# Optimization experiments

Measured on AMD Instinct MI355X. Metric: run time of the kernel, lower is better.

The kernel has to match this reference:

```python
import jax, jax.numpy as jnp
import numpy as np

N, LATENT, K, C = 50000, 16, 16, 64
BATCH = 4
MU = 2.0
HOT_TEMP = 0.01  # sigmoid temperature in hotness()


def _linear_init(key, out_dim, in_dim):
    s = 1.0 / np.sqrt(in_dim)
    kw, kb = jax.random.split(key)
    w = jax.random.uniform(kw, (out_dim, in_dim), jnp.float32, -s, s)
    b = jax.random.uniform(kb, (out_dim,), jnp.float32, -s, s)
    return w, b


def setup_inputs() -> dict:
    key = jax.random.key(0)
    ks = jax.random.split(key, 10)
    x = jax.random.normal(ks[0], (BATCH, N), jnp.float32)
    neighbour_id = jax.random.randint(ks[1], (N, K), 0, N)
    neighbour_distance = jax.random.uniform(ks[2], (N, K), jnp.float32)
    # self-neighbor at distance 0 (as in a real kNN table); keeps window sums > 0
    neighbour_distance = neighbour_distance.at[:, 0].set(0.0)
    clustering_labels = jax.random.randint(ks[3], (N,), 0, C)
    enc1_w, enc1_b = _linear_init(ks[4], 200, N)
    enc2_w, enc2_b = _linear_init(ks[5], LATENT, 200)
    dec_w, dec_b = _linear_init(ks[6], N, LATENT)
    h0_w, h0_b = _linear_init(ks[7], 200, LATENT)
    h1_w, h1_b = _linear_init(ks[8], 200, 200)
    h2_w, h2_b = _linear_init(ks[9], C, 200)
    B = jnp.array([1.0], jnp.float32)  # learnable bandwidth scale, B0=1.0
    return dict(x=x, neighbour_id=neighbour_id, neighbour_distance=neighbour_distance,
                clustering_labels=clustering_labels, enc1_w=enc1_w, enc1_b=enc1_b,
                enc2_w=enc2_w, enc2_b=enc2_b, dec_w=dec_w, dec_b=dec_b,
                h0_w=h0_w, h0_b=h0_b, h1_w=h1_w, h1_b=h1_b, h2_w=h2_w, h2_b=h2_b, B=B)


def reference(x, neighbour_id, neighbour_distance, clustering_labels,
              enc1_w, enc1_b, enc2_w, enc2_b, dec_w, dec_b,
              h0_w, h0_b, h1_w, h1_b, h2_w, h2_b, B):
    # ---- encode: Linear(N,200) -> sigmoid -> Linear(200,n)
    h = jax.nn.sigmoid(x @ enc1_w.T + enc1_b)
    encoded = h @ enc2_w.T + enc2_b                      # [b, n]

    # ---- hotness MLP (SiLU hidden layers, soft sigmoid output), batched over b
    z = encoded @ h0_w.T + h0_b
    z = z * jax.nn.sigmoid(z)
    z = z @ h1_w.T + h1_b
    z = z * jax.nn.sigmoid(z)
    z = z @ h2_w.T + h2_b                                # [b, C]
    H_cluster = jax.nn.sigmoid(HOT_TEMP * z)             # 1/(1+exp(-0.01 z))
    H = H_cluster[:, clustering_labels]                  # [b, N]

    # ---- per-mode bandwidths: (1 - H/2)^i * B,  i = 0..n-1
    powers = jnp.arange(LATENT, dtype=jnp.float32)[:, None]   # [n, 1]
    w = (1.0 - H[:, None, :] / 2.0) ** powers * B[0]          # [b, n, N]

    # ---- bubble window over K neighbours, normalized over K
    d2 = neighbour_distance ** 2                              # [N, K]
    denom = (w * MU) ** 2                                     # [b, n, N]
    win = jax.nn.relu(1.0 - d2[None, None] / denom[..., None])  # [b, n, N, K]
    win = win / jnp.sum(win, axis=-1, keepdims=True)

    # ---- convolve decoder basis (decoder.weight.T is [n, N]) with window
    basis_nbrs = dec_w.T[:, neighbour_id]                     # [n, N, K] gather
    convolved = jnp.einsum('bnik,nik->bni', win, basis_nbrs)  # [b, n, N]

    # ---- decode: bmm(encoded[b,1,n], convolved[b,n,N]) + bias
    out = jnp.einsum('bn,bni->bi', encoded, convolved) + dec_b  # [b, N]
    return out
```

## Files before the change

kernel.cpp:

```cpp
#include <hip/hip_runtime.h>
#include <math.h>

#define NPTS 50000
#define KNBR 16
#define LAT  16
#define NCLS 64
#define NB   4

#define ENC1_CHUNKS 5
#define ENC1_BLOCKS (200 * ENC1_CHUNKS)
#define NLANES (NPTS * 4)
#define CONV_BLOCKS ((NLANES + 255) / 256)

__device__ __forceinline__ float sigmoidf_(float v) { return 1.0f / (1.0f + expf(-v)); }

__global__ __launch_bounds__(256) void k_enc1(const float* __restrict__ x,
                                              const float* __restrict__ w,
                                              float* __restrict__ part) {
  const int NV4 = NPTS / 4;
  const int CV  = NV4 / ENC1_CHUNKS;
  int bid = blockIdx.x;
  int j = bid / ENC1_CHUNKS;
  int chunk = bid - j * ENC1_CHUNKS;
  int t = threadIdx.x;
  const float4* wv = (const float4*)(w + (size_t)j * NPTS);
  const float4* xv = (const float4*)x;
  float a0 = 0.f, a1 = 0.f, a2 = 0.f, a3 = 0.f;
  int vend = (chunk + 1) * CV;
#pragma unroll 2
  for (int v = chunk * CV + t; v < vend; v += 256) {
    float4 wf = wv[v];
    float4 x0 = xv[v];
    float4 x1 = xv[NV4 + v];
    float4 x2 = xv[2 * NV4 + v];
    float4 x3 = xv[3 * NV4 + v];
    a0 += wf.x * x0.x + wf.y * x0.y + wf.z * x0.z + wf.w * x0.w;
    a1 += wf.x * x1.x + wf.y * x1.y + wf.z * x1.z + wf.w * x1.w;
    a2 += wf.x * x2.x + wf.y * x2.y + wf.z * x2.z + wf.w * x2.w;
    a3 += wf.x * x3.x + wf.y * x3.y + wf.z * x3.z + wf.w * x3.w;
  }
#pragma unroll
  for (int off = 32; off > 0; off >>= 1) {
    a0 += __shfl_down(a0, off);
    a1 += __shfl_down(a1, off);
    a2 += __shfl_down(a2, off);
    a3 += __shfl_down(a3, off);
  }
  __shared__ float red[4][4];
  int wid = t >> 6;
  if ((t & 63) == 0) {
    red[wid][0] = a0; red[wid][1] = a1; red[wid][2] = a2; red[wid][3] = a3;
  }
  __syncthreads();
  if (t < 4) {
    float s = red[0][t] + red[1][t] + red[2][t] + red[3][t];
    part[j * 20 + chunk * 4 + t] = s;
  }
}

__global__ __launch_bounds__(1024) void k_mlpABC(const float* __restrict__ part,
                                                 const float* __restrict__ enc1_b,
                                                 const float* __restrict__ enc2_w,
                                                 const float* __restrict__ enc2_b,
                                                 const float* __restrict__ h0_w,
                                                 const float* __restrict__ h0_b,
                                                 float* __restrict__ w_enc,
                                                 float* __restrict__ z0g) {
  __shared__ float s_h[NB][200];
  __shared__ float s_enc[NB][LAT];
  int t = threadIdx.x;

  if (t < 800) {
    int j = t >> 2, b = t & 3;
    float v = part[j * 20 + 0 + b] + part[j * 20 + 4 + b] + part[j * 20 + 8 + b] +
              part[j * 20 + 12 + b] + part[j * 20 + 16 + b] + enc1_b[j];
    s_h[b][j] = sigmoidf_(v);
  }
  __syncthreads();

  {
    int g = t >> 4, p = t & 15;
    int b = g >> 4, i = g & 15;
    const float4* w4 = (const float4*)(enc2_w + i * 200);
    float s = 0.f;
    for (int f = p; f < 50; f += 16) {
      float4 w = w4[f];
      int j = f * 4;
      s += w.x * s_h[b][j] + w.y * s_h[b][j + 1] + w.z * s_h[b][j + 2] + w.w * s_h[b][j + 3];
    }
    s += __shfl_xor(s, 1, 16);
    s += __shfl_xor(s, 2, 16);
    s += __shfl_xor(s, 4, 16);
    s += __shfl_xor(s, 8, 16);
    if (p == 0) {
      s += enc2_b[i];
      s_enc[b][i] = s;
      w_enc[b * LAT + i] = s;
    }
  }
  __syncthreads();

  if (t < 800) {
    int jo = t >> 2, b = t & 3;
    const float4* hw = (const float4*)(h0_w + jo * LAT);
    float4 w0 = hw[0], w1 = hw[1], w2 = hw[2], w3 = hw[3];
    float s = h0_b[jo];
    s += w0.x * s_enc[b][0] + w0.y * s_enc[b][1] + w0.z * s_enc[b][2] + w0.w * s_enc[b][3];
    s += w1.x * s_enc[b][4] + w1.y * s_enc[b][5] + w1.z * s_enc[b][6] + w1.w * s_enc[b][7];
    s += w2.x * s_enc[b][8] + w2.y * s_enc[b][9] + w2.z * s_enc[b][10] + w2.w * s_enc[b][11];
    s += w3.x * s_enc[b][12] + w3.y * s_enc[b][13] + w3.z * s_enc[b][14] + w3.w * s_enc[b][15];
    z0g[jo * 4 + b] = s * sigmoidf_(s);
  }
}

__global__ __launch_bounds__(256) void k_mlpD(const float* __restrict__ z0g,
                                              const float* __restrict__ h1_w,
                                              const float* __restrict__ h1_b,
                                              float* __restrict__ z1g) {
  __shared__ __align__(16) float4 s_z0[200];
  int t = threadIdx.x;
  for (int o = t; o < 200; o += 256) s_z0[o] = ((const float4*)z0g)[o];
  __syncthreads();

  int row = blockIdx.x * 4 + (t >> 6);
  int l = t & 63;
  float d0 = 0.f, d1 = 0.f, d2 = 0.f, d3 = 0.f;
  if (l < 50) {
    float4 w = ((const float4*)(h1_w + row * 200))[l];
    float4 z0 = s_z0[4 * l + 0], z1 = s_z0[4 * l + 1];
    float4 z2 = s_z0[4 * l + 2], z3 = s_z0[4 * l + 3];
    d0 = w.x * z0.x + w.y * z1.x + w.z * z2.x + w.w * z3.x;
    d1 = w.x * z0.y + w.y * z1.y + w.z * z2.y + w.w * z3.y;
    d2 = w.x * z0.z + w.y * z1.z + w.z * z2.z + w.w * z3.z;
    d3 = w.x * z0.w + w.y * z1.w + w.z * z2.w + w.w * z3.w;
  }
#pragma unroll
  for (int m = 32; m > 0; m >>= 1) {
    d0 += __shfl_xor(d0, m, 64);
    d1 += __shfl_xor(d1, m, 64);
    d2 += __shfl_xor(d2, m, 64);
    d3 += __shfl_xor(d3, m, 64);
  }
  if (l == 0) {
    float bb = h1_b[row];
    float s;
    s = d0 + bb; z1g[row * 4 + 0] = s * sigmoidf_(s);
    s = d1 + bb; z1g[row * 4 + 1] = s * sigmoidf_(s);
    s = d2 + bb; z1g[row * 4 + 2] = s * sigmoidf_(s);
    s = d3 + bb; z1g[row * 4 + 3] = s * sigmoidf_(s);
  }
}

__global__ __launch_bounds__(256) void k_mlpE(const float* __restrict__ z1g,
                                              const float* __restrict__ h2_w,
                                              const float* __restrict__ h2_b,
                                              float* __restrict__ w_hcl) {
  __shared__ __align__(16) float4 s_z1[200];
  int t = threadIdx.x;
  for (int o = t; o < 200; o += 256) s_z1[o] = ((const float4*)z1g)[o];
  __syncthreads();

  int c = blockIdx.x * 4 + (t >> 6);
  int l = t & 63;
  float e0 = 0.f, e1 = 0.f, e2 = 0.f, e3 = 0.f;
  if (l < 50) {
    float4 w = ((const float4*)(h2_w + c * 200))[l];
    float4 za = s_z1[4 * l + 0], zb = s_z1[4 * l + 1];
    float4 zc = s_z1[4 * l + 2], zd = s_z1[4 * l + 3];
    e0 = w.x * za.x + w.y * zb.x + w.z * zc.x + w.w * zd.x;
    e1 = w.x * za.y + w.y * zb.y + w.z * zc.y + w.w * zd.y;
    e2 = w.x * za.z + w.y * zb.z + w.z * zc.z + w.w * zd.z;
    e3 = w.x * za.w + w.y * zb.w + w.z * zc.w + w.w * zd.w;
  }
#pragma unroll
  for (int m = 32; m > 0; m >>= 1) {
    e0 += __shfl_xor(e0, m, 64);
    e1 += __shfl_xor(e1, m, 64);
    e2 += __shfl_xor(e2, m, 64);
    e3 += __shfl_xor(e3, m, 64);
  }
  if (l == 0) {
    float sb = h2_b[c];
    w_hcl[0 * NCLS + c] = sigmoidf_(0.01f * (e0 + sb));
    w_hcl[1 * NCLS + c] = sigmoidf_(0.01f * (e1 + sb));
    w_hcl[2 * NCLS + c] = sigmoidf_(0.01f * (e2 + sb));
    w_hcl[3 * NCLS + c] = sigmoidf_(0.01f * (e3 + sb));
  }
}

__global__ __launch_bounds__(256) void k_conv(const int* __restrict__ nid,
                                              const float* __restrict__ nd,
                                              const int* __restrict__ labels,
                                              const float* __restrict__ dec_w,
                                              const float* __restrict__ dec_b,
                                              const float* __restrict__ Bp,
                                              const float* __restrict__ w_enc,
                                              const float* __restrict__ w_hcl,
                                              float* __restrict__ out) {
  __shared__ float s_enc[NB * LAT];
  __shared__ float s_hcl[NB * NCLS];
  int t = threadIdx.x;
  if (t < NB * LAT) s_enc[t] = w_enc[t];
  s_hcl[t] = w_hcl[t];
  __syncthreads();

  int gidx = blockIdx.x * 256 + t;
  int n = gidx >> 2;
  int q = t & 3;
  if (n >= NPTS) return;

  const float4* nd4 = (const float4*)nd + (size_t)n * 4;
  const int4*   ni4 = (const int4*)nid + (size_t)n * 4;
  float dA[16];
  int nA[16];
#pragma unroll
  for (int a = 0; a < 4; ++a) {
    float4 v = nd4[a];
    int4  iv = ni4[a];
    dA[a * 4 + 0] = v.x * v.x; dA[a * 4 + 1] = v.y * v.y;
    dA[a * 4 + 2] = v.z * v.z; dA[a * 4 + 3] = v.w * v.w;
    nA[a * 4 + 0] = iv.x; nA[a * 4 + 1] = iv.y;
    nA[a * 4 + 2] = iv.z; nA[a * 4 + 3] = iv.w;
  }

  int lab = labels[n];
  float decb = dec_b[n];
  float Bv = Bp[0];

  const float4* dw4 = (const float4*)dec_w;
  float4 dwp[8];
#pragma unroll
  for (int k = 0; k < 8; ++k)
    dwp[k] = dw4[(size_t)nA[k] * 4 + q];

  float inv0 = 1.0f / (4.0f * Bv * Bv);

  float ivd[4][4];
#pragma unroll
  for (int b = 0; b < 4; ++b) {
    float H = s_hcl[b * NCLS + lab];
    float base = 1.0f - 0.5f * H;
    float rb = __builtin_amdgcn_rcpf(base * base);
    float rb2 = rb * rb;
    float rb4 = rb2 * rb2;
    float rb8 = rb4 * rb4;
    float start = inv0;
    if (q & 1) start *= rb4;
    if (q & 2) start *= rb8;
    ivd[b][0] = start;
    ivd[b][1] = ivd[b][0] * rb;
    ivd[b][2] = ivd[b][1] * rb;
    ivd[b][3] = ivd[b][2] * rb;
  }

  float sden[4][4], num[4][4];
#pragma unroll
  for (int b = 0; b < 4; ++b)
#pragma unroll
    for (int j = 0; j < 4; ++j) { sden[b][j] = 0.f; num[b][j] = 0.f; }

#pragma unroll
  for (int k = 0; k < KNBR; ++k) {
    float4 dw = (k < 8) ? dwp[k] : dw4[(size_t)nA[k] * 4 + q];
    float d2k = dA[k];
#pragma unroll
    for (int b = 0; b < 4; ++b) {
      float w0 = fmaxf(fmaf(-d2k, ivd[b][0], 1.0f), 0.0f);
      float w1 = fmaxf(fmaf(-d2k, ivd[b][1], 1.0f), 0.0f);
      float w2 = fmaxf(fmaf(-d2k, ivd[b][2], 1.0f), 0.0f);
      float w3 = fmaxf(fmaf(-d2k, ivd[b][3], 1.0f), 0.0f);
      sden[b][0] += w0; num[b][0] = fmaf(w0, dw.x, num[b][0]);
      sden[b][1] += w1; num[b][1] = fmaf(w1, dw.y, num[b][1]);
      sden[b][2] += w2; num[b][2] = fmaf(w2, dw.z, num[b][2]);
      sden[b][3] += w3; num[b][3] = fmaf(w3, dw.w, num[b][3]);
    }
  }

  float acc[4];
#pragma unroll
  for (int b = 0; b < 4; ++b) {
    float a = 0.f;
#pragma unroll
    for (int j = 0; j < 4; ++j) {
      a = fmaf(s_enc[b * LAT + q * 4 + j] * __builtin_amdgcn_rcpf(sden[b][j]),
               num[b][j], a);
    }
    acc[b] = a;
  }

  float tA = (q & 1) ? acc[0] : acc[2];
  float tB = (q & 1) ? acc[1] : acc[3];
  float rA = __shfl_xor(tA, 1, 4);
  float rB = __shfl_xor(tB, 1, 4);
  float u = (q & 1) ? (acc[2] + rA) : (acc[0] + rA);
  float v = (q & 1) ? (acc[3] + rB) : (acc[1] + rB);
  float tC = (q & 2) ? u : v;
  float rC = __shfl_xor(tC, 2, 4);
  float f = (q & 2) ? (v + rC) : (u + rC);
  int bmap = ((q & 1) << 1) | ((q & 2) >> 1);
  out[(size_t)bmap * NPTS + n] = f + decb;
}

extern "C" void kernel_launch(void* const* d_in, const int* in_sizes, int n_in,
                              void* d_out, int out_size, void* d_ws, size_t ws_size,
                              hipStream_t stream) {
  const float* x      = (const float*)d_in[0];
  const int*   nid    = (const int*)d_in[1];
  const float* nd     = (const float*)d_in[2];
  const int*   labels = (const int*)d_in[3];
  const float* enc1_w = (const float*)d_in[4];
  const float* enc1_b = (const float*)d_in[5];
  const float* enc2_w = (const float*)d_in[6];
  const float* enc2_b = (const float*)d_in[7];
  const float* dec_w  = (const float*)d_in[8];
  const float* dec_b  = (const float*)d_in[9];
  const float* h0_w   = (const float*)d_in[10];
  const float* h0_b   = (const float*)d_in[11];
  const float* h1_w   = (const float*)d_in[12];
  const float* h1_b   = (const float*)d_in[13];
  const float* h2_w   = (const float*)d_in[14];
  const float* h2_b   = (const float*)d_in[15];
  const float* Bp     = (const float*)d_in[16];
  float* out = (float*)d_out;
  float* ws  = (float*)d_ws;
  float* part  = ws;
  float* w_enc = ws + 4000;
  float* w_hcl = ws + 4064;
  float* z0g   = ws + 4320;
  float* z1g   = ws + 5120;

  k_enc1<<<ENC1_BLOCKS, 256, 0, stream>>>(x, enc1_w, part);
  k_mlpABC<<<1, 1024, 0, stream>>>(part, enc1_b, enc2_w, enc2_b, h0_w, h0_b,
                                   w_enc, z0g);
  k_mlpD<<<50, 256, 0, stream>>>(z0g, h1_w, h1_b, z1g);
  k_mlpE<<<16, 256, 0, stream>>>(z1g, h2_w, h2_b, w_hcl);
  k_conv<<<CONV_BLOCKS, 256, 0, stream>>>(nid, nd, labels, dec_w, dec_b,
                                          Bp, w_enc, w_hcl, out);
}
```

Measured before the change: 37.76 us.

## Fuse small MLP kernels by recomputing early layers per block and final layer in conv

Merges the three small MLP launches (enc2+h0, h1, h2) into fewer kernels. Each of the 50 h1 blocks recomputes enc2 and h0 redundantly, and every conv block recomputes the h2 layer plus the hotness sigmoid from z1 before its main work. This removes two kernel launches and their serial dependency gaps. The cost is redundant arithmetic and extra h2_w reads in each of roughly 800 conv blocks.

```diff
diff --git a/kernel.cpp b/kernel.cpp
--- a/kernel.cpp
+++ b/kernel.cpp
@@ -58,20 +58,23 @@
   }
 }
 
-__global__ __launch_bounds__(1024) void k_mlpABC(const float* __restrict__ part,
-                                                 const float* __restrict__ enc1_b,
-                                                 const float* __restrict__ enc2_w,
-                                                 const float* __restrict__ enc2_b,
-                                                 const float* __restrict__ h0_w,
-                                                 const float* __restrict__ h0_b,
-                                                 float* __restrict__ w_enc,
-                                                 float* __restrict__ z0g) {
+__global__ __launch_bounds__(256) void k_mlpX(const float* __restrict__ part,
+                                              const float* __restrict__ enc1_b,
+                                              const float* __restrict__ enc2_w,
+                                              const float* __restrict__ enc2_b,
+                                              const float* __restrict__ h0_w,
+                                              const float* __restrict__ h0_b,
+                                              const float* __restrict__ h1_w,
+                                              const float* __restrict__ h1_b,
+                                              float* __restrict__ w_enc,
+                                              float* __restrict__ z1g) {
   __shared__ float s_h[NB][200];
   __shared__ float s_enc[NB][LAT];
+  __shared__ __align__(16) float s_z0t[200][NB];
   int t = threadIdx.x;
 
-  if (t < 800) {
-    int j = t >> 2, b = t & 3;
+  for (int o = t; o < 800; o += 256) {
+    int j = o >> 2, b = o & 3;
     float v = part[j * 20 + 0 + b] + part[j * 20 + 4 + b] + part[j * 20 + 8 + b] +
               part[j * 20 + 12 + b] + part[j * 20 + 16 + b] + enc1_b[j];
     s_h[b][j] = sigmoidf_(v);
@@ -79,29 +82,27 @@
   __syncthreads();
 
   {
-    int g = t >> 4, p = t & 15;
+    int g = t >> 2, p = t & 3;
     int b = g >> 4, i = g & 15;
     const float4* w4 = (const float4*)(enc2_w + i * 200);
     float s = 0.f;
-    for (int f = p; f < 50; f += 16) {
+    for (int f = p; f < 50; f += 4) {
       float4 w = w4[f];
       int j = f * 4;
       s += w.x * s_h[b][j] + w.y * s_h[b][j + 1] + w.z * s_h[b][j + 2] + w.w * s_h[b][j + 3];
     }
-    s += __shfl_xor(s, 1, 16);
-    s += __shfl_xor(s, 2, 16);
-    s += __shfl_xor(s, 4, 16);
-    s += __shfl_xor(s, 8, 16);
+    s += __shfl_xor(s, 1, 4);
+    s += __shfl_xor(s, 2, 4);
     if (p == 0) {
       s += enc2_b[i];
       s_enc[b][i] = s;
-      w_enc[b * LAT + i] = s;
-    }
-  }
-  __syncthreads();
-
-  if (t < 800) {
-    int jo = t >> 2, b = t & 3;
+      if (blockIdx.x == 0) w_enc[b * LAT + i] = s;
+    }
+  }
+  __syncthreads();
+
+  for (int o = t; o < 800; o += 256) {
+    int jo = o >> 2, b = o & 3;
     const float4* hw = (const float4*)(h0_w + jo * LAT);
     float4 w0 = hw[0], w1 = hw[1], w2 = hw[2], w3 = hw[3];
     float s = h0_b[jo];
@@ -109,82 +110,41 @@
     s += w1.x * s_enc[b][4] + w1.y * s_enc[b][5] + w1.z * s_enc[b][6] + w1.w * s_enc[b][7];
     s += w2.x * s_enc[b][8] + w2.y * s_enc[b][9] + w2.z * s_enc[b][10] + w2.w * s_enc[b][11];
     s += w3.x * s_enc[b][12] + w3.y * s_enc[b][13] + w3.z * s_enc[b][14] + w3.w * s_enc[b][15];
-    z0g[jo * 4 + b] = s * sigmoidf_(s);
-  }
-}
-
-__global__ __launch_bounds__(256) void k_mlpD(const float* __restrict__ z0g,
-                                              const float* __restrict__ h1_w,
-                                              const float* __restrict__ h1_b,
-                                              float* __restrict__ z1g) {
-  __shared__ __align__(16) float4 s_z0[200];
-  int t = threadIdx.x;
-  for (int o = t; o < 200; o += 256) s_z0[o] = ((const float4*)z0g)[o];
-  __syncthreads();
-
-  int row = blockIdx.x * 4 + (t >> 6);
-  int l = t & 63;
-  float d0 = 0.f, d1 = 0.f, d2 = 0.f, d3 = 0.f;
-  if (l < 50) {
-    float4 w = ((const float4*)(h1_w + row * 200))[l];
-    float4 z0 = s_z0[4 * l + 0], z1 = s_z0[4 * l + 1];
-    float4 z2 = s_z0[4 * l + 2], z3 = s_z0[4 * l + 3];
-    d0 = w.x * z0.x + w.y * z1.x + w.z * z2.x + w.w * z3.x;
-    d1 = w.x * z0.y + w.y * z1.y + w.z * z2.y + w.w * z3.y;
-    d2 = w.x * z0.z + w.y * z1.z + w.z * z2.z + w.w * z3.z;
-    d3 = w.x * z0.w + w.y * z1.w + w.z * z2.w + w.w * z3.w;
-  }
-#pragma unroll
-  for (int m = 32; m > 0; m >>= 1) {
-    d0 += __shfl_xor(d0, m, 64);
-    d1 += __shfl_xor(d1, m, 64);
-    d2 += __shfl_xor(d2, m, 64);
-    d3 += __shfl_xor(d3, m, 64);
-  }
-  if (l == 0) {
-    float bb = h1_b[row];
-    float s;
-    s = d0 + bb; z1g[row * 4 + 0] = s * sigmoidf_(s);
-    s = d1 + bb; z1g[row * 4 + 1] = s * sigmoidf_(s);
-    s = d2 + bb; z1g[row * 4 + 2] = s * sigmoidf_(s);
-    s = d3 + bb; z1g[row * 4 + 3] = s * sigmoidf_(s);
-  }
-}
-
-__global__ __launch_bounds__(256) void k_mlpE(const float* __restrict__ z1g,
-                                              const float* __restrict__ h2_w,
-                                              const float* __restrict__ h2_b,
-                                              float* __restrict__ w_hcl) {
-  __shared__ __align__(16) float4 s_z1[200];
-  int t = threadIdx.x;
-  for (int o = t; o < 200; o += 256) s_z1[o] = ((const float4*)z1g)[o];
-  __syncthreads();
-
-  int c = blockIdx.x * 4 + (t >> 6);
-  int l = t & 63;
-  float e0 = 0.f, e1 = 0.f, e2 = 0.f, e3 = 0.f;
-  if (l < 50) {
-    float4 w = ((const float4*)(h2_w + c * 200))[l];
-    float4 za = s_z1[4 * l + 0], zb = s_z1[4 * l + 1];
-    float4 zc = s_z1[4 * l + 2], zd = s_z1[4 * l + 3];
-    e0 = w.x * za.x + w.y * zb.x + w.z * zc.x + w.w * zd.x;
-    e1 = w.x * za.y + w.y * zb.y + w.z * zc.y + w.w * zd.y;
-    e2 = w.x * za.z + w.y * zb.z + w.z * zc.z + w.w * zd.z;
-    e3 = w.x * za.w + w.y * zb.w + w.z * zc.w + w.w * zd.w;
-  }
-#pragma unroll
-  for (int m = 32; m > 0; m >>= 1) {
-    e0 += __shfl_xor(e0, m, 64);
-    e1 += __shfl_xor(e1, m, 64);
-    e2 += __shfl_xor(e2, m, 64);
-    e3 += __shfl_xor(e3, m, 64);
-  }
-  if (l == 0) {
-    float sb = h2_b[c];
-    w_hcl[0 * NCLS + c] = sigmoidf_(0.01f * (e0 + sb));
-    w_hcl[1 * NCLS + c] = sigmoidf_(0.01f * (e1 + sb));
-    w_hcl[2 * NCLS + c] = sigmoidf_(0.01f * (e2 + sb));
-    w_hcl[3 * NCLS + c] = sigmoidf_(0.01f * (e3 + sb));
+    s_z0t[jo][b] = s * sigmoidf_(s);
+  }
+  __syncthreads();
+
+  {
+    int row = blockIdx.x * 4 + (t >> 6);
+    int l = t & 63;
+    float d0 = 0.f, d1 = 0.f, d2 = 0.f, d3 = 0.f;
+    if (l < 50) {
+      float4 w = ((const float4*)(h1_w + row * 200))[l];
+      int j = l * 4;
+      float4 z0 = *(const float4*)&s_z0t[j][0];
+      float4 z1 = *(const float4*)&s_z0t[j + 1][0];
+      float4 z2 = *(const float4*)&s_z0t[j + 2][0];
+      float4 z3 = *(const float4*)&s_z0t[j + 3][0];
+      d0 = w.x * z0.x + w.y * z1.x + w.z * z2.x + w.w * z3.x;
+      d1 = w.x * z0.y + w.y * z1.y + w.z * z2.y + w.w * z3.y;
+      d2 = w.x * z0.z + w.y * z1.z + w.z * z2.z + w.w * z3.z;
+      d3 = w.x * z0.w + w.y * z1.w + w.z * z2.w + w.w * z3.w;
+    }
+#pragma unroll
+    for (int m = 32; m > 0; m >>= 1) {
+      d0 += __shfl_xor(d0, m, 64);
+      d1 += __shfl_xor(d1, m, 64);
+      d2 += __shfl_xor(d2, m, 64);
+      d3 += __shfl_xor(d3, m, 64);
+    }
+    if (l == 0) {
+      float bb = h1_b[row];
+      float s;
+      s = d0 + bb; z1g[row * 4 + 0] = s * sigmoidf_(s);
+      s = d1 + bb; z1g[row * 4 + 1] = s * sigmoidf_(s);
+      s = d2 + bb; z1g[row * 4 + 2] = s * sigmoidf_(s);
+      s = d3 + bb; z1g[row * 4 + 3] = s * sigmoidf_(s);
+    }
   }
 }
 
@@ -195,13 +155,43 @@
                                               const float* __restrict__ dec_b,
                                               const float* __restrict__ Bp,
                                               const float* __restrict__ w_enc,
-                                              const float* __restrict__ w_hcl,
+                                              const float* __restrict__ z1g,
+                                              const float* __restrict__ h2_w,
+                                              const float* __restrict__ h2_b,
                                               float* __restrict__ out) {
   __shared__ float s_enc[NB * LAT];
   __shared__ float s_hcl[NB * NCLS];
+  __shared__ __align__(16) float4 s_z1[200];
   int t = threadIdx.x;
   if (t < NB * LAT) s_enc[t] = w_enc[t];
-  s_hcl[t] = w_hcl[t];
+  if (t < 200) s_z1[t] = ((const float4*)z1g)[t];
+  __syncthreads();
+
+  {
+    int c = t >> 2, p = t & 3;
+    const float4* w4 = (const float4*)(h2_w + c * 200);
+    float e0 = 0.f, e1 = 0.f, e2 = 0.f, e3 = 0.f;
+    for (int f = p; f < 50; f += 4) {
+      float4 w = w4[f];
+      float4 za = s_z1[f * 4 + 0], zb = s_z1[f * 4 + 1];
+      float4 zc = s_z1[f * 4 + 2], zd = s_z1[f * 4 + 3];
+      e0 += w.x * za.x + w.y * zb.x + w.z * zc.x + w.w * zd.x;
+      e1 += w.x * za.y + w.y * zb.y + w.z * zc.y + w.w * zd.y;
+      e2 += w.x * za.z + w.y * zb.z + w.z * zc.z + w.w * zd.z;
+      e3 += w.x * za.w + w.y * zb.w + w.z * zc.w + w.w * zd.w;
+    }
+    e0 += __shfl_xor(e0, 1, 4); e0 += __shfl_xor(e0, 2, 4);
+    e1 += __shfl_xor(e1, 1, 4); e1 += __shfl_xor(e1, 2, 4);
+    e2 += __shfl_xor(e2, 1, 4); e2 += __shfl_xor(e2, 2, 4);
+    e3 += __shfl_xor(e3, 1, 4); e3 += __shfl_xor(e3, 2, 4);
+    if (p == 0) {
+      float sb = h2_b[c];
+      s_hcl[0 * NCLS + c] = sigmoidf_(0.01f * (e0 + sb));
+      s_hcl[1 * NCLS + c] = sigmoidf_(0.01f * (e1 + sb));
+      s_hcl[2 * NCLS + c] = sigmoidf_(0.01f * (e2 + sb));
+      s_hcl[3 * NCLS + c] = sigmoidf_(0.01f * (e3 + sb));
+    }
+  }
   __syncthreads();
 
   int gidx = blockIdx.x * 256 + t;
@@ -325,15 +315,11 @@
   float* ws  = (float*)d_ws;
   float* part  = ws;
   float* w_enc = ws + 4000;
-  float* w_hcl = ws + 4064;
-  float* z0g   = ws + 4320;
-  float* z1g   = ws + 5120;
+  float* z1g   = ws + 4096;
 
   k_enc1<<<ENC1_BLOCKS, 256, 0, stream>>>(x, enc1_w, part);
-  k_mlpABC<<<1, 1024, 0, stream>>>(part, enc1_b, enc2_w, enc2_b, h0_w, h0_b,
-                                   w_enc, z0g);
-  k_mlpD<<<50, 256, 0, stream>>>(z0g, h1_w, h1_b, z1g);
-  k_mlpE<<<16, 256, 0, stream>>>(z1g, h2_w, h2_b, w_hcl);
+  k_mlpX<<<50, 256, 0, stream>>>(part, enc1_b, enc2_w, enc2_b, h0_w, h0_b,
+                                 h1_w, h1_b, w_enc, z1g);
   k_conv<<<CONV_BLOCKS, 256, 0, stream>>>(nid, nd, labels, dec_w, dec_b,
-                                          Bp, w_enc, w_hcl, out);
+                                          Bp, w_enc, z1g, h2_w, h2_b, out);
 }
```

New measurement: 42.67 us. 13.0% more time.
